# Optimization experiments

Measured on AMD Instinct MI355X. Metric: run time of the kernel, lower is better.

## Reference

```python
import jax, jax.numpy as jnp
import numpy as np

N = 30000        # num nodes
R = 16           # num relations
B = 30           # num bases (hard-coded in source)
E = 960000       # num edges (avg degree 32)
IN, HID, OUT, ADR = 128, 128, 64, 400


def setup_inputs() -> dict:
    key = jax.random.key(0)
    ks = jax.random.split(key, 13)
    s_in = 1.0 / np.sqrt(IN)
    s_hid = 1.0 / np.sqrt(HID)
    s_out = 1.0 / np.sqrt(OUT)
    return {
        "x": jax.random.normal(ks[0], (N, IN), jnp.float32),
        "edge_index": jax.random.randint(ks[1], (2, E), 0, N, jnp.int64),
        "edge_type": jax.random.randint(ks[2], (E,), 0, R, jnp.int64),
        "comp1": jax.random.normal(ks[3], (R, B), jnp.float32) * (1.0 / np.sqrt(B)),
        "basis1": jax.random.normal(ks[4], (B, IN, HID), jnp.float32) * s_in,
        "root1": jax.random.normal(ks[5], (IN, HID), jnp.float32) * s_in,
        "bias1": jnp.zeros((HID,), jnp.float32),
        "comp2": jax.random.normal(ks[6], (R, B), jnp.float32) * (1.0 / np.sqrt(B)),
        "basis2": jax.random.normal(ks[7], (B, HID, OUT), jnp.float32) * s_hid,
        "root2": jax.random.normal(ks[8], (HID, OUT), jnp.float32) * s_hid,
        "bias2": jnp.zeros((OUT,), jnp.float32),
        "wc": jax.random.normal(ks[9], (OUT, ADR), jnp.float32) * s_out,
        "bc": jnp.zeros((ADR,), jnp.float32),
    }


def _rgcn_conv(x, src, dst, etype, comp, basis, root, bias):
    """PyG RGCNConv: out[i] = sum_r mean_{e: dst=i, rel=r} x[src_e] @ W_r + x[i] @ root + bias,
    with basis decomposition W_r = sum_b comp[r,b] * basis[b].
    Aggregate-first: segment-mean x[src] into (node, relation) buckets, then contract."""
    n, din = x.shape
    seg = dst * R + etype                                   # [E] composite segment id
    msg = x[src]                                            # [E, din] edge gather
    sums = jax.ops.segment_sum(msg, seg, num_segments=n * R)            # [N*R, din]
    cnt = jax.ops.segment_sum(jnp.ones((src.shape[0],), x.dtype), seg,
                              num_segments=n * R)                       # [N*R]
    mean = sums / jnp.maximum(cnt, 1.0)[:, None]            # per-relation mean
    agg = mean.reshape(n, R, din)                           # [N, R, din]
    w = jnp.einsum('rb,bio->rio', comp, basis)              # [R, din, dout]
    return jnp.einsum('nri,rio->no', agg, w) + x @ root + bias


def reference(x, edge_index, edge_type, comp1, basis1, root1, bias1,
              comp2, basis2, root2, bias2, wc, bc):
    src, dst = edge_index[0], edge_index[1]
    h = _rgcn_conv(x, src, dst, edge_type, comp1, basis1, root1, bias1)
    h = jax.nn.relu(h)
    h = _rgcn_conv(h, src, dst, edge_type, comp2, basis2, root2, bias2)
    return h @ wc + bc
```

## Files before the change

### kernel.cpp

```cpp
#include <hip/hip_runtime.h>

#define R_    16
#define NBAS  30
#define DIN1  128
#define DHID  128
#define DOUT2 64
#define DADR  400
#define KCH   128
#define LDB   ((R_ + 1) * 128)

typedef __attribute__((ext_vector_type(8))) short bf16x8;
typedef __attribute__((ext_vector_type(4))) float f32x4;

__device__ __forceinline__ short f2bf(float f) {
    unsigned u = __float_as_uint(f);
    u += 0x7fffu + ((u >> 16) & 1u);
    return (short)(u >> 16);
}
__device__ __forceinline__ unsigned packbf(float lo, float hi) {
    return (unsigned)(unsigned short)f2bf(lo) | ((unsigned)(unsigned short)f2bf(hi) << 16);
}

struct Row8 { f32x4 lo, hi; };

__device__ __forceinline__ Row8 row8_zero() {
    Row8 z; z.lo = (f32x4){0.f,0.f,0.f,0.f}; z.hi = (f32x4){0.f,0.f,0.f,0.f}; return z;
}
__device__ __forceinline__ Row8 row8_add(Row8 a, int4 v) {
    unsigned u0 = (unsigned)v.x, u1 = (unsigned)v.y, u2 = (unsigned)v.z, u3 = (unsigned)v.w;
    a.lo[0] += __uint_as_float(u0 << 16);
    a.lo[1] += __uint_as_float(u0 & 0xffff0000u);
    a.lo[2] += __uint_as_float(u1 << 16);
    a.lo[3] += __uint_as_float(u1 & 0xffff0000u);
    a.hi[0] += __uint_as_float(u2 << 16);
    a.hi[1] += __uint_as_float(u2 & 0xffff0000u);
    a.hi[2] += __uint_as_float(u3 << 16);
    a.hi[3] += __uint_as_float(u3 & 0xffff0000u);
    return a;
}
__device__ __forceinline__ int4 row8_pack(Row8 a) {
    int4 o;
    o.x = (int)packbf(a.lo[0], a.lo[1]);
    o.y = (int)packbf(a.lo[2], a.lo[3]);
    o.z = (int)packbf(a.hi[0], a.hi[1]);
    o.w = (int)packbf(a.hi[2], a.hi[3]);
    return o;
}

__device__ __forceinline__ Row8 gather_idx(const short* __restrict__ featbf,
                                           const int* __restrict__ srt,
                                           int b, int c, int idx, int l16) {
    Row8 a = row8_zero();
    int s = c < 16 ? c : 16;
    int j = 0;
    for (; j + 4 <= s; j += 4) {
        int i0 = __shfl(idx, j, 16);
        int i1 = __shfl(idx, j + 1, 16);
        int i2 = __shfl(idx, j + 2, 16);
        int i3 = __shfl(idx, j + 3, 16);
        int4 v0 = *(const int4*)(featbf + (size_t)i0 * KCH + l16 * 8);
        int4 v1 = *(const int4*)(featbf + (size_t)i1 * KCH + l16 * 8);
        int4 v2 = *(const int4*)(featbf + (size_t)i2 * KCH + l16 * 8);
        int4 v3 = *(const int4*)(featbf + (size_t)i3 * KCH + l16 * 8);
        a = row8_add(a, v0); a = row8_add(a, v1);
        a = row8_add(a, v2); a = row8_add(a, v3);
    }
    for (; j + 2 <= s; j += 2) {
        int i0 = __shfl(idx, j, 16);
        int i1 = __shfl(idx, j + 1, 16);
        int4 v0 = *(const int4*)(featbf + (size_t)i0 * KCH + l16 * 8);
        int4 v1 = *(const int4*)(featbf + (size_t)i1 * KCH + l16 * 8);
        a = row8_add(a, v0); a = row8_add(a, v1);
    }
    if (j < s) {
        int i0 = __shfl(idx, j, 16);
        a = row8_add(a, *(const int4*)(featbf + (size_t)i0 * KCH + l16 * 8));
    }
    for (int p = b + 16; p < b + c; ++p)
        a = row8_add(a, *(const int4*)(featbf + (size_t)srt[p] * KCH + l16 * 8));
    float sc = 1.f / (float)(c > 1 ? c : 1);
    a.lo *= sc; a.hi *= sc;
    return a;
}

__global__ __launch_bounds__(256) void tobf_kernel(const float* __restrict__ in,
                                                   short* __restrict__ out, int n4) {
    int i = blockIdx.x * 256 + threadIdx.x;
    if (i >= n4) return;
    float4 v = ((const float4*)in)[i];
    short4 b = { f2bf(v.x), f2bf(v.y), f2bf(v.z), f2bf(v.w) };
    ((short4*)out)[i] = b;
}

__global__ __launch_bounds__(256) void count_kernel(const int* __restrict__ dst,
                                                    const int* __restrict__ ety,
                                                    int* __restrict__ cnt, int E, int N) {
    int e = blockIdx.x * blockDim.x + threadIdx.x;
    if (e < E) atomicAdd(&cnt[ety[e] * N + dst[e]], 1);
}

#define SCAN_CHUNK 2048
#define SCAN_IT    8

__global__ __launch_bounds__(256) void scan_bsum_kernel(const int* __restrict__ cnt, int nseg,
                                                        int* __restrict__ bsum) {
    __shared__ int sd[256];
    int base = blockIdx.x * SCAN_CHUNK;
    int s = 0;
    #pragma unroll
    for (int j = 0; j < SCAN_IT; ++j) {
        int idx = base + j * 256 + threadIdx.x;
        if (idx < nseg) s += cnt[idx];
    }
    sd[threadIdx.x] = s;
    __syncthreads();
    for (int st = 128; st > 0; st >>= 1) {
        if (threadIdx.x < st) sd[threadIdx.x] += sd[threadIdx.x + st];
        __syncthreads();
    }
    if (threadIdx.x == 0) bsum[blockIdx.x] = sd[0];
}

__global__ __launch_bounds__(256) void scan_top_kernel(const int* __restrict__ bsum, int nblk,
                                                       int* __restrict__ boff,
                                                       int* __restrict__ off, int nseg) {
    if (nblk > 256) {
        if (threadIdx.x == 0) {
            int run = 0;
            for (int i = 0; i < nblk; ++i) { int t = bsum[i]; boff[i] = run; run += t; }
            off[nseg] = run;
        }
        return;
    }
    __shared__ int sd[256];
    int v = (threadIdx.x < nblk) ? bsum[threadIdx.x] : 0;
    sd[threadIdx.x] = v;
    __syncthreads();
    for (int st = 1; st < 256; st <<= 1) {
        int t = (threadIdx.x >= st) ? sd[threadIdx.x - st] : 0;
        __syncthreads();
        sd[threadIdx.x] += t;
        __syncthreads();
    }
    if (threadIdx.x < nblk) boff[threadIdx.x] = sd[threadIdx.x] - v;
    if (threadIdx.x == nblk - 1) off[nseg] = sd[threadIdx.x];
}

__global__ __launch_bounds__(256) void scan_final_kernel(const int* __restrict__ cnt, int nseg,
                                                         const int* __restrict__ boff,
                                                         int* __restrict__ off,
                                                         int* __restrict__ cursor) {
    __shared__ int sd[256];
    int base = blockIdx.x * SCAN_CHUNK + threadIdx.x * SCAN_IT;
    int v[SCAN_IT];
    int s = 0;
    #pragma unroll
    for (int j = 0; j < SCAN_IT; ++j) {
        int idx = base + j;
        v[j] = (idx < nseg) ? cnt[idx] : 0;
        s += v[j];
    }
    sd[threadIdx.x] = s;
    __syncthreads();
    for (int st = 1; st < 256; st <<= 1) {
        int t = (threadIdx.x >= st) ? sd[threadIdx.x - st] : 0;
        __syncthreads();
        sd[threadIdx.x] += t;
        __syncthreads();
    }
    int run = boff[blockIdx.x] + sd[threadIdx.x] - s;
    #pragma unroll
    for (int j = 0; j < SCAN_IT; ++j) {
        int idx = base + j;
        if (idx < nseg) { off[idx] = run; cursor[idx] = run; }
        run += v[j];
    }
}

__global__ __launch_bounds__(256) void reorder_kernel(const int* __restrict__ src,
                                                      const int* __restrict__ dst,
                                                      const int* __restrict__ ety,
                                                      int* __restrict__ cursor,
                                                      int* __restrict__ srt, int E, int N) {
    int e = blockIdx.x * blockDim.x + threadIdx.x;
    if (e >= E) return;
    int seg = ety[e] * N + dst[e];
    int pos = atomicAdd(&cursor[seg], 1);
    srt[pos] = src[e];
}

#define PREP1 (R_ * DIN1 * DHID)
#define PREP2 (PREP1 + R_ * DHID * DOUT2)
#define PREP3 (PREP2 + DIN1 * DHID)
#define PREP4 (PREP3 + DHID * DOUT2)
#define PREP5 (PREP4 + DADR * DOUT2)
__global__ __launch_bounds__(256) void prep_kernel(const float* __restrict__ comp1,
                                                   const float* __restrict__ basis1,
                                                   const float* __restrict__ root1,
                                                   const float* __restrict__ comp2,
                                                   const float* __restrict__ basis2,
                                                   const float* __restrict__ root2,
                                                   const float* __restrict__ wc,
                                                   short* __restrict__ BT1,
                                                   short* __restrict__ BT2,
                                                   short* __restrict__ wcT) {
    int idx = blockIdx.x * 256 + threadIdx.x;
    if (idx < PREP1) {
        int o = idx % DHID, i = (idx / DHID) % DIN1, r = idx / (DHID * DIN1);
        float acc = 0.f;
        #pragma unroll 6
        for (int b = 0; b < NBAS; ++b)
            acc += comp1[r * NBAS + b] * basis1[((size_t)b * DIN1 + i) * DHID + o];
        BT1[(size_t)o * LDB + r * DIN1 + i] = f2bf(acc);
    } else if (idx < PREP2) {
        int t = idx - PREP1;
        int o = t % DOUT2, i = (t / DOUT2) % DHID, r = t / (DOUT2 * DHID);
        float acc = 0.f;
        #pragma unroll 6
        for (int b = 0; b < NBAS; ++b)
            acc += comp2[r * NBAS + b] * basis2[((size_t)b * DHID + i) * DOUT2 + o];
        BT2[(size_t)o * LDB + r * DHID + i] = f2bf(acc);
    } else if (idx < PREP3) {
        int t = idx - PREP2;
        int o = t % DHID, i = t / DHID;
        BT1[(size_t)o * LDB + R_ * DIN1 + i] = f2bf(root1[(size_t)i * DHID + o]);
    } else if (idx < PREP4) {
        int t = idx - PREP3;
        int o = t % DOUT2, i = t / DOUT2;
        BT2[(size_t)o * LDB + R_ * DHID + i] = f2bf(root2[(size_t)i * DOUT2 + o]);
    } else if (idx < PREP5) {
        int t = idx - PREP4;
        int a = t / DOUT2, k = t % DOUT2;
        wcT[(size_t)a * DOUT2 + k] = f2bf(wc[(size_t)k * DADR + a]);
    }
}

template<int BN, bool OUTBF>
__global__ __launch_bounds__(256, 4)
void rgcn_fused_kernel(const short* __restrict__ featbf,
                       const int* __restrict__ off2,
                       const int* __restrict__ srt,
                       const short* __restrict__ BT,
                       const float* __restrict__ bias,
                       void* __restrict__ Hout, int N, int relu)
{
    constexpr int BM = 32, BK = 128;
    constexpr int WN = BN / 4;
    constexpr int MR = 2;
    constexpr int NR = WN / 16;
    constexpr int BL = BN / 16;

    __shared__ short lA[BM * BK];
    __shared__ short lB[BN * BK];

    const int tid  = threadIdx.x;
    const int lane = tid & 63;
    const int wv   = tid >> 6;
    const int g16  = tid >> 4;
    const int l16  = tid & 15;
    const int n0   = blockIdx.x * BM;
    const int row0 = n0 + g16;
    const int row1 = n0 + 16 + g16;

    f32x4 acc[MR][NR];
    #pragma unroll
    for (int m = 0; m < MR; ++m)
        #pragma unroll
        for (int n = 0; n < NR; ++n)
            acc[m][n] = (f32x4){0.f, 0.f, 0.f, 0.f};

    int b0v = 0, e0v = 0, b1v = 0, e1v = 0;
    if (row0 < N) { b0v = off2[l16 * N + row0]; e0v = off2[l16 * N + row0 + 1]; }
    if (row1 < N) { b1v = off2[l16 * N + row1]; e1v = off2[l16 * N + row1 + 1]; }

    int cb0 = __shfl(b0v, 0, 16), cc0 = __shfl(e0v, 0, 16) - cb0;
    int cb1 = __shfl(b1v, 0, 16), cc1 = __shfl(e1v, 0, 16) - cb1;
    int cidx0 = (l16 < (cc0 < 16 ? cc0 : 16)) ? srt[cb0 + l16] : 0;
    int cidx1 = (l16 < (cc1 < 16 ? cc1 : 16)) ? srt[cb1 + l16] : 0;

    for (int r = 0; r <= R_; ++r) {
        __syncthreads();

        int4 vb[BL];
        #pragma unroll
        for (int j = 0; j < BL; ++j)
            vb[j] = *(const int4*)(BT + (size_t)(j * 16 + g16) * LDB + r * BK + l16 * 8);

        int nb0 = 0, nc0 = 0, nb1 = 0, nc1 = 0, nidx0 = 0, nidx1 = 0;
        if (r + 1 < R_) {
            nb0 = __shfl(b0v, r + 1, 16); nc0 = __shfl(e0v, r + 1, 16) - nb0;
            nb1 = __shfl(b1v, r + 1, 16); nc1 = __shfl(e1v, r + 1, 16) - nb1;
            nidx0 = (l16 < (nc0 < 16 ? nc0 : 16)) ? srt[nb0 + l16] : 0;
            nidx1 = (l16 < (nc1 < 16 ? nc1 : 16)) ? srt[nb1 + l16] : 0;
        }

        Row8 a0, a1;
        if (r < R_) {
            a0 = gather_idx(featbf, srt, cb0, cc0, cidx0, l16);
            a1 = gather_idx(featbf, srt, cb1, cc1, cidx1, l16);
        } else {
            a0 = row8_zero(); a1 = row8_zero();
            if (row0 < N)
                a0 = row8_add(a0, *(const int4*)(featbf + (size_t)row0 * KCH + l16 * 8));
            if (row1 < N)
                a1 = row8_add(a1, *(const int4*)(featbf + (size_t)row1 * KCH + l16 * 8));
        }

        {
            int byte0 = ((g16 * BK + l16 * 8) << 1) ^ ((g16 & 15) << 4);
            *(int4*)((char*)lA + byte0) = row8_pack(a0);
            int rowl = 16 + g16;
            int byte1 = ((rowl * BK + l16 * 8) << 1) ^ ((rowl & 15) << 4);
            *(int4*)((char*)lA + byte1) = row8_pack(a1);
        }
        #pragma unroll
        for (int j = 0; j < BL; ++j) {
            int o = j * 16 + g16;
            int byte = ((o * BK + l16 * 8) << 1) ^ ((o & 15) << 4);
            *(int4*)((char*)lB + byte) = vb[j];
        }
        __syncthreads();

        #pragma unroll
        for (int kk = 0; kk < BK / 32; ++kk) {
            const int kpos = kk * 32 + (lane >> 4) * 8;
            bf16x8 af[MR], bfr[NR];
            #pragma unroll
            for (int m = 0; m < MR; ++m) {
                int row = m * 16 + (lane & 15);
                af[m] = *(const bf16x8*)((const char*)lA +
                         (((row * BK + kpos) << 1) ^ ((row & 15) << 4)));
            }
            #pragma unroll
            for (int n = 0; n < NR; ++n) {
                int col = wv * WN + n * 16 + (lane & 15);
                bfr[n] = *(const bf16x8*)((const char*)lB +
                         (((col * BK + kpos) << 1) ^ ((col & 15) << 4)));
            }
            #pragma unroll
            for (int m = 0; m < MR; ++m)
                #pragma unroll
                for (int n = 0; n < NR; ++n)
                    acc[m][n] = __builtin_amdgcn_mfma_f32_16x16x32_bf16(
                        af[m], bfr[n], acc[m][n], 0, 0, 0);
        }

        cb0 = nb0; cc0 = nc0; cidx0 = nidx0;
        cb1 = nb1; cc1 = nc1; cidx1 = nidx1;
    }

    #pragma unroll
    for (int m = 0; m < MR; ++m)
        #pragma unroll
        for (int n = 0; n < NR; ++n)
            #pragma unroll
            for (int i = 0; i < 4; ++i) {
                int row  = m * 16 + ((lane >> 4) << 2) + i;
                int col  = wv * WN + n * 16 + (lane & 15);
                int grow = n0 + row;
                if (grow >= N) continue;
                float v = acc[m][n][i] + bias[col];
                if (relu) v = fmaxf(v, 0.f);
                if (OUTBF) ((short*)Hout)[(size_t)grow * BN + col] = f2bf(v);
                else       ((float*)Hout)[(size_t)grow * BN + col] = v;
            }
}

__global__ __launch_bounds__(256)
void classifier_gemm_kernel(const short* __restrict__ h2bf,
                            const short* __restrict__ wcT,
                            const float* __restrict__ bc,
                            float* __restrict__ out, int N)
{
    constexpr int BM = 128, BN = 80, BK = 64;
    constexpr int MR = 2, NR = 5;

    __shared__ short lA[BM * BK];
    __shared__ short lB[BN * BK];

    const int tid  = threadIdx.x;
    const int lane = tid & 63;
    const int wv   = tid >> 6;
    const int nodeBase = blockIdx.x * BM;
    const int colBase  = blockIdx.y * BN;

    const int t8  = tid & 7;
    const int r32 = tid >> 3;

    #pragma unroll
    for (int it = 0; it < 4; ++it) {
        int row  = it * 32 + r32;
        int grow = nodeBase + row;
        int4 v = {0, 0, 0, 0};
        if (grow < N) v = *(const int4*)(h2bf + (size_t)grow * DOUT2 + t8 * 8);
        int byte = ((row * BK + t8 * 8) << 1) ^ ((row & 7) << 4);
        *(int4*)((char*)lA + byte) = v;
    }
    for (int o = r32; o < BN; o += 32) {
        int4 v = *(const int4*)(wcT + (size_t)(colBase + o) * DOUT2 + t8 * 8);
        int byte = ((o * BK + t8 * 8) << 1) ^ ((o & 7) << 4);
        *(int4*)((char*)lB + byte) = v;
    }
    __syncthreads();

    f32x4 acc[MR][NR];
    #pragma unroll
    for (int m = 0; m < MR; ++m)
        #pragma unroll
        for (int n = 0; n < NR; ++n)
            acc[m][n] = (f32x4){0.f, 0.f, 0.f, 0.f};

    #pragma unroll
    for (int kk = 0; kk < BK / 32; ++kk) {
        const int kpos = kk * 32 + (lane >> 4) * 8;
        bf16x8 af[MR], bfr[NR];
        #pragma unroll
        for (int m = 0; m < MR; ++m) {
            int row = wv * 32 + m * 16 + (lane & 15);
            af[m] = *(const bf16x8*)((const char*)lA +
                     (((row * BK + kpos) << 1) ^ ((row & 7) << 4)));
        }
        #pragma unroll
        for (int n = 0; n < NR; ++n) {
            int col = n * 16 + (lane & 15);
            bfr[n] = *(const bf16x8*)((const char*)lB +
                     (((col * BK + kpos) << 1) ^ ((col & 7) << 4)));
        }
        #pragma unroll
        for (int m = 0; m < MR; ++m)
            #pragma unroll
            for (int n = 0; n < NR; ++n)
                acc[m][n] = __builtin_amdgcn_mfma_f32_16x16x32_bf16(
                    af[m], bfr[n], acc[m][n], 0, 0, 0);
    }

    #pragma unroll
    for (int m = 0; m < MR; ++m)
        #pragma unroll
        for (int n = 0; n < NR; ++n)
            #pragma unroll
            for (int i = 0; i < 4; ++i) {
                int row  = wv * 32 + m * 16 + ((lane >> 4) << 2) + i;
                int col  = n * 16 + (lane & 15);
                int grow = nodeBase + row;
                if (grow >= N) continue;
                int gcol = colBase + col;
                out[(size_t)grow * DADR + gcol] = acc[m][n][i] + bc[gcol];
            }
}

static inline size_t align16(size_t x) { return (x + 15) & ~(size_t)15; }

extern "C" void kernel_launch(void* const* d_in, const int* in_sizes, int n_in,
                              void* d_out, int out_size, void* d_ws, size_t ws_size,
                              hipStream_t stream) {
    const float* x      = (const float*)d_in[0];
    const int*   ei     = (const int*)d_in[1];
    const int*   et     = (const int*)d_in[2];
    const float* comp1  = (const float*)d_in[3];
    const float* basis1 = (const float*)d_in[4];
    const float* root1  = (const float*)d_in[5];
    const float* bias1  = (const float*)d_in[6];
    const float* comp2  = (const float*)d_in[7];
    const float* basis2 = (const float*)d_in[8];
    const float* root2  = (const float*)d_in[9];
    const float* bias2  = (const float*)d_in[10];
    const float* wc     = (const float*)d_in[11];
    const float* bc     = (const float*)d_in[12];
    float* out = (float*)d_out;

    const int E = in_sizes[1] / 2;
    const int N = in_sizes[0] / DIN1;
    const int* srcp = ei;
    const int* dstp = ei + E;

    const int NSEG = N * R_;
    const int NBLK = (NSEG + SCAN_CHUNK - 1) / SCAN_CHUNK;

    char* ws = (char*)d_ws;
    size_t o = 0;
    int*   cntI   = (int*)(ws + o);   o = align16(o + (size_t)NSEG * 4);
    int*   off2   = (int*)(ws + o);   o = align16(o + (size_t)(NSEG + 1) * 4);
    int*   cursor = (int*)(ws + o);   o = align16(o + (size_t)NSEG * 4);
    int*   bsum   = (int*)(ws + o);   o = align16(o + (size_t)NBLK * 4);
    int*   boff   = (int*)(ws + o);   o = align16(o + (size_t)NBLK * 4);
    int*   srt    = (int*)(ws + o);   o = align16(o + (size_t)E * 4);
    short* BT1    = (short*)(ws + o); o = align16(o + (size_t)DHID * LDB * 2);
    short* BT2    = (short*)(ws + o); o = align16(o + (size_t)DOUT2 * LDB * 2);
    short* wcTb   = (short*)(ws + o); o = align16(o + (size_t)DADR * DOUT2 * 2);
    short* xbf    = (short*)(ws + o); o = align16(o + (size_t)N * DIN1 * 2);
    short* h1bf   = (short*)(ws + o); o = align16(o + (size_t)N * DHID * 2);
    short* h2bf   = (short*)(ws + o); o = align16(o + (size_t)N * DOUT2 * 2);

    const int n4 = N * DIN1 / 4;
    tobf_kernel<<<(n4 + 255) / 256, 256, 0, stream>>>(x, xbf, n4);

    hipMemsetAsync(cntI, 0, (size_t)NSEG * 4, stream);
    count_kernel<<<(E + 255) / 256, 256, 0, stream>>>(dstp, et, cntI, E, N);
    scan_bsum_kernel<<<NBLK, 256, 0, stream>>>(cntI, NSEG, bsum);
    scan_top_kernel<<<1, 256, 0, stream>>>(bsum, NBLK, boff, off2, NSEG);
    scan_final_kernel<<<NBLK, 256, 0, stream>>>(cntI, NSEG, boff, off2, cursor);
    reorder_kernel<<<(E + 255) / 256, 256, 0, stream>>>(srcp, dstp, et, cursor, srt, E, N);

    prep_kernel<<<(PREP5 + 255) / 256, 256, 0, stream>>>(comp1, basis1, root1,
                                                         comp2, basis2, root2, wc,
                                                         BT1, BT2, wcTb);

    const int gGrid = (N + 31) / 32;
    rgcn_fused_kernel<DHID, true><<<gGrid, 256, 0, stream>>>(xbf,  off2, srt, BT1, bias1, h1bf, N, 1);
    rgcn_fused_kernel<DOUT2, true><<<gGrid, 256, 0, stream>>>(h1bf, off2, srt, BT2, bias2, h2bf, N, 0);

    dim3 cGrid((N + 127) / 128, DADR / 80);
    classifier_gemm_kernel<<<cGrid, 256, 0, stream>>>(h2bf, wcTb, bc, out, N);
}
```

Before: 297.4 us.

## Software-pipeline first four neighbor row gathers one relation ahead of MFMA

Restructures the relation loop so that the first four neighbor feature rows for the next relation are loaded into registers before the MFMA phase of the current relation. Index lookups move two relations ahead. The root (self) row is folded in as a one-element bucket at r == R_. This is meant to hide gather latency behind compute. The cost is more live registers (16 int4 buffers), which may reduce occupancy, and buckets with more than four edges still do their extra loads serially.

New measurement: 308.7 us. 1.04x slower.

```diff
diff --git a/kernel.cpp b/kernel.cpp
--- a/kernel.cpp
+++ b/kernel.cpp
@@ -45,42 +45,6 @@
     o.z = (int)packbf(a.hi[0], a.hi[1]);
     o.w = (int)packbf(a.hi[2], a.hi[3]);
     return o;
-}
-
-__device__ __forceinline__ Row8 gather_idx(const short* __restrict__ featbf,
-                                           const int* __restrict__ srt,
-                                           int b, int c, int idx, int l16) {
-    Row8 a = row8_zero();
-    int s = c < 16 ? c : 16;
-    int j = 0;
-    for (; j + 4 <= s; j += 4) {
-        int i0 = __shfl(idx, j, 16);
-        int i1 = __shfl(idx, j + 1, 16);
-        int i2 = __shfl(idx, j + 2, 16);
-        int i3 = __shfl(idx, j + 3, 16);
-        int4 v0 = *(const int4*)(featbf + (size_t)i0 * KCH + l16 * 8);
-        int4 v1 = *(const int4*)(featbf + (size_t)i1 * KCH + l16 * 8);
-        int4 v2 = *(const int4*)(featbf + (size_t)i2 * KCH + l16 * 8);
-        int4 v3 = *(const int4*)(featbf + (size_t)i3 * KCH + l16 * 8);
-        a = row8_add(a, v0); a = row8_add(a, v1);
-        a = row8_add(a, v2); a = row8_add(a, v3);
-    }
-    for (; j + 2 <= s; j += 2) {
-        int i0 = __shfl(idx, j, 16);
-        int i1 = __shfl(idx, j + 1, 16);
-        int4 v0 = *(const int4*)(featbf + (size_t)i0 * KCH + l16 * 8);
-        int4 v1 = *(const int4*)(featbf + (size_t)i1 * KCH + l16 * 8);
-        a = row8_add(a, v0); a = row8_add(a, v1);
-    }
-    if (j < s) {
-        int i0 = __shfl(idx, j, 16);
-        a = row8_add(a, *(const int4*)(featbf + (size_t)i0 * KCH + l16 * 8));
-    }
-    for (int p = b + 16; p < b + c; ++p)
-        a = row8_add(a, *(const int4*)(featbf + (size_t)srt[p] * KCH + l16 * 8));
-    float sc = 1.f / (float)(c > 1 ? c : 1);
-    a.lo *= sc; a.hi *= sc;
-    return a;
 }
 
 __global__ __launch_bounds__(256) void tobf_kernel(const float* __restrict__ in,
@@ -278,6 +242,22 @@
     int cidx0 = (l16 < (cc0 < 16 ? cc0 : 16)) ? srt[cb0 + l16] : 0;
     int cidx1 = (l16 < (cc1 < 16 ? cc1 : 16)) ? srt[cb1 + l16] : 0;
 
+    int4 sc0[4], sc1[4], sn0[4], sn1[4];
+    #pragma unroll
+    for (int j = 0; j < 4; ++j) {
+        int i0 = __shfl(cidx0, j, 16);
+        sc0[j] = (j < cc0) ? *(const int4*)(featbf + (size_t)i0 * KCH + l16 * 8)
+                           : (int4){0, 0, 0, 0};
+        int i1 = __shfl(cidx1, j, 16);
+        sc1[j] = (j < cc1) ? *(const int4*)(featbf + (size_t)i1 * KCH + l16 * 8)
+                           : (int4){0, 0, 0, 0};
+    }
+
+    int nb0 = __shfl(b0v, 1, 16), nc0 = __shfl(e0v, 1, 16) - nb0;
+    int nb1 = __shfl(b1v, 1, 16), nc1 = __shfl(e1v, 1, 16) - nb1;
+    int nidx0 = (l16 < (nc0 < 16 ? nc0 : 16)) ? srt[nb0 + l16] : 0;
+    int nidx1 = (l16 < (nc1 < 16 ? nc1 : 16)) ? srt[nb1 + l16] : 0;
+
     for (int r = 0; r <= R_; ++r) {
         __syncthreads();
 
@@ -286,24 +266,47 @@
         for (int j = 0; j < BL; ++j)
             vb[j] = *(const int4*)(BT + (size_t)(j * 16 + g16) * LDB + r * BK + l16 * 8);
 
-        int nb0 = 0, nc0 = 0, nb1 = 0, nc1 = 0, nidx0 = 0, nidx1 = 0;
-        if (r + 1 < R_) {
-            nb0 = __shfl(b0v, r + 1, 16); nc0 = __shfl(e0v, r + 1, 16) - nb0;
-            nb1 = __shfl(b1v, r + 1, 16); nc1 = __shfl(e1v, r + 1, 16) - nb1;
-            nidx0 = (l16 < (nc0 < 16 ? nc0 : 16)) ? srt[nb0 + l16] : 0;
-            nidx1 = (l16 < (nc1 < 16 ? nc1 : 16)) ? srt[nb1 + l16] : 0;
-        }
-
-        Row8 a0, a1;
-        if (r < R_) {
-            a0 = gather_idx(featbf, srt, cb0, cc0, cidx0, l16);
-            a1 = gather_idx(featbf, srt, cb1, cc1, cidx1, l16);
-        } else {
-            a0 = row8_zero(); a1 = row8_zero();
-            if (row0 < N)
-                a0 = row8_add(a0, *(const int4*)(featbf + (size_t)row0 * KCH + l16 * 8));
-            if (row1 < N)
-                a1 = row8_add(a1, *(const int4*)(featbf + (size_t)row1 * KCH + l16 * 8));
+        int pb0 = 0, pc0 = 0, pidx0 = 0, pb1 = 0, pc1 = 0, pidx1 = 0;
+        {
+            int rr = r + 2;
+            if (rr < R_) {
+                pb0 = __shfl(b0v, rr, 16); pc0 = __shfl(e0v, rr, 16) - pb0;
+                pb1 = __shfl(b1v, rr, 16); pc1 = __shfl(e1v, rr, 16) - pb1;
+                pidx0 = (l16 < (pc0 < 16 ? pc0 : 16)) ? srt[pb0 + l16] : 0;
+                pidx1 = (l16 < (pc1 < 16 ? pc1 : 16)) ? srt[pb1 + l16] : 0;
+            } else if (rr == R_) {
+                pc0 = (row0 < N) ? 1 : 0; pidx0 = (row0 < N) ? row0 : 0;
+                pc1 = (row1 < N) ? 1 : 0; pidx1 = (row1 < N) ? row1 : 0;
+            }
+        }
+
+        Row8 a0 = row8_zero(), a1 = row8_zero();
+        #pragma unroll
+        for (int j = 0; j < 4; ++j) {
+            if (j < cc0) a0 = row8_add(a0, sc0[j]);
+            if (j < cc1) a1 = row8_add(a1, sc1[j]);
+        }
+        if (cc0 > 4) {
+            for (int j = 4; j < cc0 && j < 16; ++j) {
+                int i0 = __shfl(cidx0, j, 16);
+                a0 = row8_add(a0, *(const int4*)(featbf + (size_t)i0 * KCH + l16 * 8));
+            }
+            for (int p = cb0 + 16; p < cb0 + cc0; ++p)
+                a0 = row8_add(a0, *(const int4*)(featbf + (size_t)srt[p] * KCH + l16 * 8));
+        }
+        if (cc1 > 4) {
+            for (int j = 4; j < cc1 && j < 16; ++j) {
+                int i1 = __shfl(cidx1, j, 16);
+                a1 = row8_add(a1, *(const int4*)(featbf + (size_t)i1 * KCH + l16 * 8));
+            }
+            for (int p = cb1 + 16; p < cb1 + cc1; ++p)
+                a1 = row8_add(a1, *(const int4*)(featbf + (size_t)srt[p] * KCH + l16 * 8));
+        }
+        {
+            float s0 = 1.f / (float)(cc0 > 1 ? cc0 : 1);
+            a0.lo *= s0; a0.hi *= s0;
+            float s1 = 1.f / (float)(cc1 > 1 ? cc1 : 1);
+            a1.lo *= s1; a1.hi *= s1;
         }
 
         {
@@ -319,6 +322,18 @@
             int byte = ((o * BK + l16 * 8) << 1) ^ ((o & 15) << 4);
             *(int4*)((char*)lB + byte) = vb[j];
         }
+
+        if (r < R_) {
+            #pragma unroll
+            for (int j = 0; j < 4; ++j) {
+                int i0 = __shfl(nidx0, j, 16);
+                sn0[j] = (j < nc0) ? *(const int4*)(featbf + (size_t)i0 * KCH + l16 * 8)
+                                   : (int4){0, 0, 0, 0};
+                int i1 = __shfl(nidx1, j, 16);
+                sn1[j] = (j < nc1) ? *(const int4*)(featbf + (size_t)i1 * KCH + l16 * 8)
+                                   : (int4){0, 0, 0, 0};
+            }
+        }
         __syncthreads();
 
         #pragma unroll
@@ -347,6 +362,10 @@
 
         cb0 = nb0; cc0 = nc0; cidx0 = nidx0;
         cb1 = nb1; cc1 = nc1; cidx1 = nidx1;
+        nb0 = pb0; nc0 = pc0; nidx0 = pidx0;
+        nb1 = pb1; nc1 = pc1; nidx1 = pidx1;
+        #pragma unroll
+        for (int j = 0; j < 4; ++j) { sc0[j] = sn0[j]; sc1[j] = sn1[j]; }
     }
 
     #pragma unroll
```

## Prestore weights in LDS-swizzled layout and load via global_load_lds; merge setup kernels

Applied to the files above, without the earlier changes.

Weight-prep now writes the combined relation weights in a per-relation, pre-swizzled layout that matches the LDS tile. The fused RGCN kernel can then copy each B tile straight into shared memory with global_load_lds, skipping the register round trip and the swizzled ds_write. The bf16 conversion of x, edge counting and weight prep are also merged into one setup kernel to cut launch count. This relies on the direct-to-LDS copy offsets matching the swizzle exactly, and the merged kernel mixes different kinds of work in one grid.

After: 295.3 us, median of 2. No clear change (-0.7%).

```diff
diff --git a/kernel.cpp b/kernel.cpp
--- a/kernel.cpp
+++ b/kernel.cpp
@@ -7,7 +7,6 @@
 #define DOUT2 64
 #define DADR  400
 #define KCH   128
-#define LDB   ((R_ + 1) * 128)
 
 typedef __attribute__((ext_vector_type(8))) short bf16x8;
 typedef __attribute__((ext_vector_type(4))) float f32x4;
@@ -45,6 +44,17 @@
     o.z = (int)packbf(a.hi[0], a.hi[1]);
     o.w = (int)packbf(a.hi[2], a.hi[3]);
     return o;
+}
+
+__device__ __forceinline__ void gload_lds16(const void* g, void* l) {
+    __builtin_amdgcn_global_load_lds(
+        (const __attribute__((address_space(1))) unsigned int*)g,
+        (__attribute__((address_space(3))) unsigned int*)l, 16, 0, 0);
+}
+
+__device__ __forceinline__ size_t swzidx(int r, int o, int k, int chStride) {
+    int ib = ((o * 256 + ((k >> 3) << 4)) ^ ((o & 15) << 4)) + ((k & 7) << 1);
+    return (size_t)r * chStride + (ib >> 1);
 }
 
 __device__ __forceinline__ Row8 gather_idx(const short* __restrict__ featbf,
@@ -83,20 +93,63 @@
     return a;
 }
 
-__global__ __launch_bounds__(256) void tobf_kernel(const float* __restrict__ in,
-                                                   short* __restrict__ out, int n4) {
-    int i = blockIdx.x * 256 + threadIdx.x;
-    if (i >= n4) return;
-    float4 v = ((const float4*)in)[i];
-    short4 b = { f2bf(v.x), f2bf(v.y), f2bf(v.z), f2bf(v.w) };
-    ((short4*)out)[i] = b;
-}
-
-__global__ __launch_bounds__(256) void count_kernel(const int* __restrict__ dst,
-                                                    const int* __restrict__ ety,
-                                                    int* __restrict__ cnt, int E, int N) {
-    int e = blockIdx.x * blockDim.x + threadIdx.x;
-    if (e < E) atomicAdd(&cnt[ety[e] * N + dst[e]], 1);
+#define PREP1 (R_ * DIN1 * DHID)
+#define PREP2 (PREP1 + R_ * DHID * DOUT2)
+#define PREP3 (PREP2 + DIN1 * DHID)
+#define PREP4 (PREP3 + DHID * DOUT2)
+#define PREP5 (PREP4 + DADR * DOUT2)
+__global__ __launch_bounds__(256)
+void setup_kernel(const float* __restrict__ x, short* __restrict__ xbf, int n4,
+                  const int* __restrict__ dst, const int* __restrict__ ety,
+                  int* __restrict__ cnt, int E, int N,
+                  const float* __restrict__ comp1, const float* __restrict__ basis1,
+                  const float* __restrict__ root1,
+                  const float* __restrict__ comp2, const float* __restrict__ basis2,
+                  const float* __restrict__ root2,
+                  const float* __restrict__ wc,
+                  short* __restrict__ BT1, short* __restrict__ BT2,
+                  short* __restrict__ wcT) {
+    int gid = blockIdx.x * 256 + threadIdx.x;
+    if (gid < n4) {
+        float4 v = ((const float4*)x)[gid];
+        short4 b = { f2bf(v.x), f2bf(v.y), f2bf(v.z), f2bf(v.w) };
+        ((short4*)xbf)[gid] = b;
+        return;
+    }
+    gid -= n4;
+    if (gid < E) {
+        atomicAdd(&cnt[ety[gid] * N + dst[gid]], 1);
+        return;
+    }
+    int idx = gid - E;
+    if (idx < PREP1) {
+        int o = idx % DHID, i = (idx / DHID) % DIN1, r = idx / (DHID * DIN1);
+        float acc = 0.f;
+        #pragma unroll 6
+        for (int b = 0; b < NBAS; ++b)
+            acc += comp1[r * NBAS + b] * basis1[((size_t)b * DIN1 + i) * DHID + o];
+        BT1[swzidx(r, o, i, DHID * 128)] = f2bf(acc);
+    } else if (idx < PREP2) {
+        int t = idx - PREP1;
+        int o = t % DOUT2, i = (t / DOUT2) % DHID, r = t / (DOUT2 * DHID);
+        float acc = 0.f;
+        #pragma unroll 6
+        for (int b = 0; b < NBAS; ++b)
+            acc += comp2[r * NBAS + b] * basis2[((size_t)b * DHID + i) * DOUT2 + o];
+        BT2[swzidx(r, o, i, DOUT2 * 128)] = f2bf(acc);
+    } else if (idx < PREP3) {
+        int t = idx - PREP2;
+        int o = t % DHID, i = t / DHID;
+        BT1[swzidx(R_, o, i, DHID * 128)] = f2bf(root1[(size_t)i * DHID + o]);
+    } else if (idx < PREP4) {
+        int t = idx - PREP3;
+        int o = t % DOUT2, i = t / DOUT2;
+        BT2[swzidx(R_, o, i, DOUT2 * 128)] = f2bf(root2[(size_t)i * DOUT2 + o]);
+    } else if (idx < PREP5) {
+        int t = idx - PREP4;
+        int a = t / DOUT2, k = t % DOUT2;
+        wcT[(size_t)a * DOUT2 + k] = f2bf(wc[(size_t)k * DADR + a]);
+    }
 }
 
 #define SCAN_CHUNK 2048
@@ -187,52 +240,6 @@
     int seg = ety[e] * N + dst[e];
     int pos = atomicAdd(&cursor[seg], 1);
     srt[pos] = src[e];
-}
-
-#define PREP1 (R_ * DIN1 * DHID)
-#define PREP2 (PREP1 + R_ * DHID * DOUT2)
-#define PREP3 (PREP2 + DIN1 * DHID)
-#define PREP4 (PREP3 + DHID * DOUT2)
-#define PREP5 (PREP4 + DADR * DOUT2)
-__global__ __launch_bounds__(256) void prep_kernel(const float* __restrict__ comp1,
-                                                   const float* __restrict__ basis1,
-                                                   const float* __restrict__ root1,
-                                                   const float* __restrict__ comp2,
-                                                   const float* __restrict__ basis2,
-                                                   const float* __restrict__ root2,
-                                                   const float* __restrict__ wc,
-                                                   short* __restrict__ BT1,
-                                                   short* __restrict__ BT2,
-                                                   short* __restrict__ wcT) {
-    int idx = blockIdx.x * 256 + threadIdx.x;
-    if (idx < PREP1) {
-        int o = idx % DHID, i = (idx / DHID) % DIN1, r = idx / (DHID * DIN1);
-        float acc = 0.f;
-        #pragma unroll 6
-        for (int b = 0; b < NBAS; ++b)
-            acc += comp1[r * NBAS + b] * basis1[((size_t)b * DIN1 + i) * DHID + o];
-        BT1[(size_t)o * LDB + r * DIN1 + i] = f2bf(acc);
-    } else if (idx < PREP2) {
-        int t = idx - PREP1;
-        int o = t % DOUT2, i = (t / DOUT2) % DHID, r = t / (DOUT2 * DHID);
-        float acc = 0.f;
-        #pragma unroll 6
-        for (int b = 0; b < NBAS; ++b)
-            acc += comp2[r * NBAS + b] * basis2[((size_t)b * DHID + i) * DOUT2 + o];
-        BT2[(size_t)o * LDB + r * DHID + i] = f2bf(acc);
-    } else if (idx < PREP3) {
-        int t = idx - PREP2;
-        int o = t % DHID, i = t / DHID;
-        BT1[(size_t)o * LDB + R_ * DIN1 + i] = f2bf(root1[(size_t)i * DHID + o]);
-    } else if (idx < PREP4) {
-        int t = idx - PREP3;
-        int o = t % DOUT2, i = t / DOUT2;
-        BT2[(size_t)o * LDB + R_ * DHID + i] = f2bf(root2[(size_t)i * DOUT2 + o]);
-    } else if (idx < PREP5) {
-        int t = idx - PREP4;
-        int a = t / DOUT2, k = t % DOUT2;
-        wcT[(size_t)a * DOUT2 + k] = f2bf(wc[(size_t)k * DADR + a]);
-    }
 }
 
 template<int BN, bool OUTBF>
@@ -248,7 +255,7 @@
     constexpr int WN = BN / 4;
     constexpr int MR = 2;
     constexpr int NR = WN / 16;
-    constexpr int BL = BN / 16;
+    constexpr int NCOPY = BN / 16;
 
     __shared__ short lA[BM * BK];
     __shared__ short lB[BN * BK];
@@ -281,10 +288,15 @@
     for (int r = 0; r <= R_; ++r) {
         __syncthreads();
 
-        int4 vb[BL];
-        #pragma unroll
-        for (int j = 0; j < BL; ++j)
-            vb[j] = *(const int4*)(BT + (size_t)(j * 16 + g16) * LDB + r * BK + l16 * 8);
+        {
+            const char* srcB = (const char*)BT + (size_t)r * BN * 256;
+            #pragma unroll
+            for (int j = 0; j < NCOPY; ++j) {
+                const char* g = srcB + j * 4096 + wv * 1024 + (lane << 4);
+                char* l = (char*)lB + j * 4096 + wv * 1024;
+                gload_lds16(g, l);
+            }
+        }
 
         int nb0 = 0, nc0 = 0, nb1 = 0, nc1 = 0, nidx0 = 0, nidx1 = 0;
         if (r + 1 < R_) {
@@ -312,12 +324,6 @@
             int rowl = 16 + g16;
             int byte1 = ((rowl * BK + l16 * 8) << 1) ^ ((rowl & 15) << 4);
             *(int4*)((char*)lA + byte1) = row8_pack(a1);
-        }
-        #pragma unroll
-        for (int j = 0; j < BL; ++j) {
-            int o = j * 16 + g16;
-            int byte = ((o * BK + l16 * 8) << 1) ^ ((o & 15) << 4);
-            *(int4*)((char*)lB + byte) = vb[j];
         }
         __syncthreads();
 
@@ -485,27 +491,29 @@
     int*   bsum   = (int*)(ws + o);   o = align16(o + (size_t)NBLK * 4);
     int*   boff   = (int*)(ws + o);   o = align16(o + (size_t)NBLK * 4);
     int*   srt    = (int*)(ws + o);   o = align16(o + (size_t)E * 4);
-    short* BT1    = (short*)(ws + o); o = align16(o + (size_t)DHID * LDB * 2);
-    short* BT2    = (short*)(ws + o); o = align16(o + (size_t)DOUT2 * LDB * 2);
+    short* BT1    = (short*)(ws + o); o = align16(o + (size_t)(R_ + 1) * DHID * 128 * 2);
+    short* BT2    = (short*)(ws + o); o = align16(o + (size_t)(R_ + 1) * DOUT2 * 128 * 2);
     short* wcTb   = (short*)(ws + o); o = align16(o + (size_t)DADR * DOUT2 * 2);
     short* xbf    = (short*)(ws + o); o = align16(o + (size_t)N * DIN1 * 2);
     short* h1bf   = (short*)(ws + o); o = align16(o + (size_t)N * DHID * 2);
     short* h2bf   = (short*)(ws + o); o = align16(o + (size_t)N * DOUT2 * 2);
 
     const int n4 = N * DIN1 / 4;
-    tobf_kernel<<<(n4 + 255) / 256, 256, 0, stream>>>(x, xbf, n4);
-
     hipMemsetAsync(cntI, 0, (size_t)NSEG * 4, stream);
-    count_kernel<<<(E + 255) / 256, 256, 0, stream>>>(dstp, et, cntI, E, N);
+    {
+        long long total = (long long)n4 + E + PREP5;
+        int grid = (int)((total + 255) / 256);
+        setup_kernel<<<grid, 256, 0, stream>>>(x, xbf, n4, dstp, et, cntI, E, N,
+                                               comp1, basis1, root1,
+                                               comp2, basis2, root2, wc,
+                                               BT1, BT2, wcTb);
+    }
+
     scan_bsum_kernel<<<NBLK, 256, 0, stream>>>(cntI, NSEG, bsum);
     scan_top_kernel<<<1, 256, 0, stream>>>(bsum, NBLK, boff, off2, NSEG);
     scan_final_kernel<<<NBLK, 256, 0, stream>>>(cntI, NSEG, boff, off2, cursor);
     reorder_kernel<<<(E + 255) / 256, 256, 0, stream>>>(srcp, dstp, et, cursor, srt, E, N);
 
-    prep_kernel<<<(PREP5 + 255) / 256, 256, 0, stream>>>(comp1, basis1, root1,
-                                                         comp2, basis2, root2, wc,
-                                                         BT1, BT2, wcTb);
-
     const int gGrid = (N + 31) / 32;
     rgcn_fused_kernel<DHID, true><<<gGrid, 256, 0, stream>>>(xbf,  off2, srt, BT1, bias1, h1bf, N, 1);
     rgcn_fused_kernel<DOUT2, true><<<gGrid, 256, 0, stream>>>(h1bf, off2, srt, BT2, bias2, h2bf, N, 0);
```
